# Performance work log

Measured on AMD Instinct MI355X. Metric: run time of the kernel, lower is better.

## Reference

```python
import jax, jax.numpy as jnp
import numpy as np

NEG_INF = jnp.finfo(jnp.float32).min


def _continual_mask(attach_test_after, Q, K, test_num, chunk_size):
    """Boolean allowed-mask [B, 1, Q, K] replicating get_continual_mask +
    the per-batch test-query/train-key override in forward()."""
    k_train = K - test_num * chunk_size
    q_train = Q - test_num * chunk_size
    qi = jnp.arange(Q)[:, None]          # [Q,1]
    kj = jnp.arange(K)[None, :]          # [1,K]
    # base causal mask with diagonal offset K-Q (train queries)
    base = kj <= qi + (K - Q)            # [Q,K]
    # block-diagonal tril for test-query / test-key region
    dq = qi - q_train                    # local test row (negative for train rows, unused there)
    dk = kj - k_train
    block = (kj >= k_train) & (dk <= dq) & ((dk // chunk_size) == (dq // chunk_size))
    # per-batch: test query in chunk n may see train keys <= attach_test_after[b, n]
    chunk_idx = jnp.clip(dq[:, 0], 0, None) // chunk_size          # [Q]
    att = attach_test_after[:, chunk_idx]                          # [B,Q]
    train_key_allowed = kj[None, :, :] <= att[:, :, None]          # [B,Q,K]
    allowed = jnp.where(qi < q_train, base[None],
                        jnp.where(kj[None] < k_train, train_key_allowed, block[None]))
    return allowed[:, None]              # [B,1,Q,K]


def setup_inputs() -> dict:
    key = jax.random.key(0)
    k1, k2, k3, k4 = jax.random.split(key, 4)
    B, L, H, D = 4, 2048, 8, 64
    test_num, train_len = 64, 1536
    return {
        "queries": jax.random.normal(k1, (B, L, H, D), dtype=jnp.float32),
        "keys": jax.random.normal(k2, (B, L, H, D), dtype=jnp.float32),
        "values": jax.random.normal(k3, (B, L, H, D), dtype=jnp.float32),
        "attach_test_after": jax.random.randint(k4, (B, test_num), 0, train_len).astype(jnp.int64),
        "train_len": train_len,
    }


def reference(queries, keys, values, attach_test_after, train_len):
    B, Lq, H, Dqk = queries.shape
    test_num = attach_test_after.shape[1]
    chunk_size = (Lq - train_len) // test_num
    q = jnp.transpose(queries, (0, 2, 1, 3))   # [B,H,Lq,D]
    k = jnp.transpose(keys, (0, 2, 1, 3))      # [B,H,Lk,D]
    v = jnp.transpose(values, (0, 2, 1, 3))    # [B,H,Lk,Dv]
    Lk = k.shape[2]
    # vanilla path: scaled QK^T + continual mask + softmax + AV
    logits = jnp.einsum('bhmd,bhnd->bhmn', q, k) / jnp.sqrt(jnp.float32(Dqk))
    allowed = _continual_mask(attach_test_after, Lq, Lk, test_num, chunk_size)
    logits = jnp.where(allowed, logits, NEG_INF)
    attn = jax.nn.softmax(logits, axis=-1)
    out = jnp.einsum('bhmn,bhnd->bhmd', attn, v)
    return out.transpose(0, 2, 1, 3).reshape(B, Lq, H * v.shape[-1])  # b l (h d)
```

## Files before the change

### kernel.cpp

```cpp
#include <hip/hip_runtime.h>
#include <hip/hip_bf16.h>

typedef __bf16 bf16_t;
typedef __bf16 bf16x8 __attribute__((ext_vector_type(8)));
typedef float  f32x4  __attribute__((ext_vector_type(4)));

#define MFMA16(a, b, c) __builtin_amdgcn_mfma_f32_16x16x32_bf16((a), (b), (c), 0, 0, 0)

constexpr int Bc = 4, Lc = 2048, Hc = 8, Dc = 64;
constexpr int HD = Hc * Dc;
constexpr int TRAINc = 1536;
constexpr int ROWS_BLK = 64;
constexpr int KT = 64;

constexpr int PREPK_BLOCKS = (int)((size_t)Bc * Lc * Hc * Dc / 8 / 256);

__global__ void prep_fused(const float* __restrict__ K, bf16_t* __restrict__ Kb,
                           const float* __restrict__ V, bf16_t* __restrict__ Vt) {
  __shared__ bf16_t T[64][64];
  const int t = (int)threadIdx.x;

  if ((int)blockIdx.x < PREPK_BLOCKS) {
    size_t g = ((size_t)blockIdx.x * 256 + t) * 8;
    float4 a = *(const float4*)(K + g);
    float4 b = *(const float4*)(K + g + 4);
    bf16x8 v;
    v[0] = (bf16_t)a.x; v[1] = (bf16_t)a.y; v[2] = (bf16_t)a.z; v[3] = (bf16_t)a.w;
    v[4] = (bf16_t)b.x; v[5] = (bf16_t)b.y; v[6] = (bf16_t)b.z; v[7] = (bf16_t)b.w;
    *(bf16x8*)(Kb + g) = v;
    return;
  }

  const int bid = (int)blockIdx.x - PREPK_BLOCKS;
  const int kt = bid & 31, h = (bid >> 5) & 7, b = bid >> 8;
  {
    int kl = t >> 2, dp = (t & 3) << 4;
    const float* s = V + ((size_t)(b * Lc + kt * 64 + kl) * Hc + h) * Dc + dp;
    bf16x8 v0, v1;
    float4 f;
    f = *(const float4*)(s);      v0[0]=(bf16_t)f.x; v0[1]=(bf16_t)f.y; v0[2]=(bf16_t)f.z; v0[3]=(bf16_t)f.w;
    f = *(const float4*)(s + 4);  v0[4]=(bf16_t)f.x; v0[5]=(bf16_t)f.y; v0[6]=(bf16_t)f.z; v0[7]=(bf16_t)f.w;
    f = *(const float4*)(s + 8);  v1[0]=(bf16_t)f.x; v1[1]=(bf16_t)f.y; v1[2]=(bf16_t)f.z; v1[3]=(bf16_t)f.w;
    f = *(const float4*)(s + 12); v1[4]=(bf16_t)f.x; v1[5]=(bf16_t)f.y; v1[6]=(bf16_t)f.z; v1[7]=(bf16_t)f.w;
    const int x = kl >> 3;
    const int c0 = dp >> 3;
    *(bf16x8*)&T[kl][(c0 ^ x) << 3]       = v0;
    *(bf16x8*)&T[kl][((c0 + 1) ^ x) << 3] = v1;
  }
  __syncthreads();
  {
    int d = t >> 2, kp = (t & 3) << 4;
    const int xa = kp >> 3;
    const int xb = xa + 1;
    const int lo = d & 7, hi = d >> 3;
    const int x0 = ((hi ^ xa) << 3) + lo;
    const int x1 = ((hi ^ xb) << 3) + lo;
    bf16x8 o0, o1;
#pragma unroll
    for (int i = 0; i < 8; ++i) { o0[i] = T[kp + i][x0]; o1[i] = T[kp + 8 + i][x1]; }
    bf16_t* dst = Vt + ((size_t)((b * Hc + h) * Dc + d)) * Lc + kt * 64 + kp;
    *(bf16x8*)dst = o0;
    *(bf16x8*)(dst + 8) = o1;
  }
}

static __device__ __forceinline__ void load16(const bf16_t* g, bf16_t* l) {
  __builtin_amdgcn_global_load_lds(
      (const __attribute__((address_space(1))) unsigned int*)g,
      (__attribute__((address_space(3))) unsigned int*)l, 16, 0, 0);
}

static __device__ __forceinline__ bf16x8 mk8(unsigned w0, unsigned w1,
                                             unsigned w2, unsigned w3) {
  union { unsigned u[4]; bf16x8 v; } x;
  x.u[0] = w0; x.u[1] = w1; x.u[2] = w2; x.u[3] = w3;
  return x.v;
}

__global__ __launch_bounds__(256, 4)
void continual_attn(const float* __restrict__ Qg, const bf16_t* __restrict__ Kb,
                    const bf16_t* __restrict__ Vt, const int* __restrict__ ATT,
                    float* __restrict__ OUT)
{
  __shared__ __align__(16) bf16_t Klds[2][KT * 64];
  __shared__ __align__(16) bf16_t Vlds[2][Dc * KT];

  const int bid  = blockIdx.x;
  const int qblk = 31 - (bid >> 5);
  const int h    = bid & 7;
  const int b    = (bid >> 3) & 3;
  const int q0   = qblk * ROWS_BLK;

  const int tid  = (int)threadIdx.x;
  const int wave = tid >> 6;
  const int lane = tid & 63;
  const int quad = lane >> 4;
  const int col  = lane & 15;
  const int qw   = q0 + wave * 16;

  const size_t bhQ = (size_t)b * Lc * HD + (size_t)h * Dc;

  const int kr = tid >> 3;
  const bf16_t* ksrcA = Kb + bhQ + (size_t)kr * HD + (((tid & 7) ^ (kr & 7)) << 3);
  const bf16_t* vsrcA = Vt + ((size_t)((b * Hc + h) * Dc + kr)) * Lc + (((tid & 7) ^ (kr & 7)) << 3);
  const bf16_t* vsrcB = vsrcA + (size_t)32 * Lc;

  bf16x8 aq[2];
  {
    const float* qp = Qg + bhQ + (size_t)(qw + col) * HD + quad * 8;
    const float SC = 0.125f * 1.44269504f;
#pragma unroll
    for (int t = 0; t < 2; ++t) {
      float4 lo = *(const float4*)(qp + t * 32);
      float4 hi = *(const float4*)(qp + t * 32 + 4);
      bf16x8 v;
      v[0] = (bf16_t)(lo.x * SC); v[1] = (bf16_t)(lo.y * SC);
      v[2] = (bf16_t)(lo.z * SC); v[3] = (bf16_t)(lo.w * SC);
      v[4] = (bf16_t)(hi.x * SC); v[5] = (bf16_t)(hi.y * SC);
      v[6] = (bf16_t)(hi.z * SC); v[7] = (bf16_t)(hi.w * SC);
      aq[t] = v;
    }
  }

  const bool testblk = (q0 >= TRAINc);
  const int qi = qw + col;
  int kendL, cstartL;
  if (testblk) {
    kendL   = ATT[b * 64 + ((qi - TRAINc) >> 3)] + 1;
    cstartL = qi & ~7;
  } else {
    kendL   = qi + 1;
    cstartL = 0;
  }

  int ntA, ndiag, kfull_end;
  if (testblk) {
    int c0 = (q0 - TRAINc) >> 3;
    int amax = 0, amin = 0x7fffffff;
#pragma unroll
    for (int i = 0; i < 8; ++i) {
      int a = ATT[b * 64 + c0 + i];
      amax = (a > amax) ? a : amax;
      amin = (a < amin) ? a : amin;
    }
    ntA = (amax >> 6) + 1;
    ndiag = 1;
    kfull_end = amin + 1;
  } else {
    ntA = qblk + 1;
    ndiag = 0;
    kfull_end = q0 + 1;
  }
  const int ntot = ntA + ndiag;

  float ls[4] = {0.f, 0.f, 0.f, 0.f};
  f32x4 o[4] = {{0,0,0,0},{0,0,0,0},{0,0,0,0},{0,0,0,0}};

  const int cA = ((quad ^ (col & 7)) << 3);

  {
    bf16_t* kd = Klds[0];
    bf16_t* vd = Vlds[0];
    load16(ksrcA, kd + wave * 512);
    load16(ksrcA + (size_t)32 * HD, kd + 2048 + wave * 512);
    load16(vsrcA, vd + wave * 512);
    load16(vsrcB, vd + 2048 + wave * 512);
  }

  for (int ti = 0; ti < ntot; ++ti) {
    const int buf = ti & 1;
    __syncthreads();

    if (ti + 1 < ntot) {
      const int kn = (ti + 1 < ntA) ? (ti + 1) * KT : q0 + (ti + 1 - ntA) * KT;
      bf16_t* kd = Klds[1 - buf];
      bf16_t* vd = Vlds[1 - buf];
      load16(ksrcA + (size_t)kn * HD, kd + wave * 512);
      load16(ksrcA + (size_t)(kn + 32) * HD, kd + 2048 + wave * 512);
      load16(vsrcA + kn, vd + wave * 512);
      load16(vsrcB + kn, vd + 2048 + wave * 512);
    }

    const bf16_t* kb = Klds[buf];
    const bf16_t* vbuf = Vlds[buf];
    const int k0 = (ti < ntA) ? ti * KT : q0 + (ti - ntA) * KT;

    f32x4 sf[4] = {{0,0,0,0},{0,0,0,0},{0,0,0,0},{0,0,0,0}};
    __builtin_amdgcn_s_setprio(1);
#pragma unroll
    for (int kg = 0; kg < 4; ++kg) {
      const bf16_t* krow = kb + (kg * 16 + col) * 64;
      bf16x8 k0f = *(const bf16x8*)(krow + cA);
      bf16x8 k1f = *(const bf16x8*)(krow + (cA ^ 32));
      sf[kg] = MFMA16(k0f, aq[0], sf[kg]);
      sf[kg] = MFMA16(k1f, aq[1], sf[kg]);
    }
    __builtin_amdgcn_s_setprio(0);

    const int mode = (ti >= ntA) ? 2 : ((k0 + KT <= kfull_end) ? 0 : 1);
    if (mode == 1) {
#pragma unroll
      for (int kg = 0; kg < 4; ++kg) {
        const int kv = k0 + kg * 16 + quad * 4;
#pragma unroll
        for (int r = 0; r < 4; ++r)
          if (kv + r >= kendL) sf[kg][r] = -1e30f;
      }
    } else if (mode == 2) {
#pragma unroll
      for (int kg = 0; kg < 4; ++kg) {
        const int kv = k0 + kg * 16 + quad * 4;
#pragma unroll
        for (int r = 0; r < 4; ++r)
          if (kv + r < cstartL || kv + r > qi) sf[kg][r] = -1e30f;
      }
    }

    float pvv[4][4];
#pragma unroll
    for (int kg = 0; kg < 4; ++kg)
#pragma unroll
      for (int r = 0; r < 4; ++r) {
        float p = __builtin_amdgcn_exp2f(sf[kg][r]);
        pvv[kg][r] = p;
        ls[r] += p;
      }

    unsigned Dw[4][2];
#pragma unroll
    for (int kg = 0; kg < 4; ++kg)
#pragma unroll
      for (int d = 0; d < 2; ++d)
        asm("v_cvt_pk_bf16_f32 %0, %1, %2"
            : "=v"(Dw[kg][d]) : "v"(pvv[kg][2 * d]), "v"(pvv[kg][2 * d + 1]));

    unsigned a0 = Dw[0][0], b0 = Dw[1][0];
    asm volatile("v_permlane32_swap_b32 %0, %1" : "+v"(a0), "+v"(b0));
    asm volatile("v_permlane16_swap_b32 %0, %1" : "+v"(a0), "+v"(b0));
    unsigned a1 = Dw[0][1], b1 = Dw[1][1];
    asm volatile("v_permlane32_swap_b32 %0, %1" : "+v"(a1), "+v"(b1));
    asm volatile("v_permlane16_swap_b32 %0, %1" : "+v"(a1), "+v"(b1));
    unsigned a2 = Dw[2][0], b2 = Dw[3][0];
    asm volatile("v_permlane32_swap_b32 %0, %1" : "+v"(a2), "+v"(b2));
    asm volatile("v_permlane16_swap_b32 %0, %1" : "+v"(a2), "+v"(b2));
    unsigned a3 = Dw[2][1], b3 = Dw[3][1];
    asm volatile("v_permlane32_swap_b32 %0, %1" : "+v"(a3), "+v"(b3));
    asm volatile("v_permlane16_swap_b32 %0, %1" : "+v"(a3), "+v"(b3));

    bf16x8 pa0 = mk8(a0, a1, b0, b1);
    bf16x8 pa1 = mk8(a2, a3, b2, b3);

    __builtin_amdgcn_s_setprio(1);
#pragma unroll
    for (int t = 0; t < 4; ++t) {
      const bf16_t* vrow = vbuf + (t * 16 + col) * 64;
      bf16x8 v0 = *(const bf16x8*)(vrow + cA);
      bf16x8 v1 = *(const bf16x8*)(vrow + (cA ^ 32));
      o[t] = MFMA16(pa0, v0, o[t]);
      o[t] = MFMA16(pa1, v1, o[t]);
    }
    __builtin_amdgcn_s_setprio(0);
  }

  float rs = (ls[0] + ls[1]) + (ls[2] + ls[3]);
  rs += __shfl_xor(rs, 16);
  rs += __shfl_xor(rs, 32);
#pragma unroll
  for (int r = 0; r < 4; ++r) {
    float dr = __shfl(rs, quad * 4 + r);
    float inv = 1.f / dr;
    int qo = qw + quad * 4 + r;
    float* op = OUT + ((size_t)b * Lc + qo) * HD + (size_t)h * Dc + col;
    op[0]  = o[0][r] * inv;
    op[16] = o[1][r] * inv;
    op[32] = o[2][r] * inv;
    op[48] = o[3][r] * inv;
  }
}

extern "C" void kernel_launch(void* const* d_in, const int* in_sizes, int n_in,
                              void* d_out, int out_size, void* d_ws, size_t ws_size,
                              hipStream_t stream) {
  const float* Q   = (const float*)d_in[0];
  const float* K   = (const float*)d_in[1];
  const float* V   = (const float*)d_in[2];
  const int*   ATT = (const int*)d_in[3];
  float* OUT = (float*)d_out;
  (void)in_sizes; (void)n_in; (void)out_size; (void)ws_size;

  const size_t NE = (size_t)Bc * Lc * Hc * Dc;
  bf16_t* Kb = (bf16_t*)d_ws;
  bf16_t* Vt = Kb + NE;

  prep_fused<<<dim3((unsigned)(PREPK_BLOCKS + Bc * Hc * (Lc / 64))), dim3(256), 0, stream>>>(K, Kb, V, Vt);
  continual_attn<<<dim3(Bc * Hc * (Lc / ROWS_BLK)), dim3(256), 0, stream>>>(Q, Kb, Vt, ATT, OUT);
}
```

Before: 126.7 us.

## Load K/V tiles directly from global into registers, drop LDS staging

Replaces the double-buffered LDS staging of K and V tiles (global_load_lds plus block barriers) with per-wave direct global loads into registers feeding the MFMAs. It also reorders the q-block schedule so heavy and light causal blocks are interleaved across the grid. This removes LDS traffic and __syncthreads, but each of the four waves now fetches the same K/V data separately, and with no prefetch the load latency is exposed inside each iteration.

```diff
diff --git a/kernel.cpp b/kernel.cpp
--- a/kernel.cpp
+++ b/kernel.cpp
@@ -64,12 +64,6 @@
   }
 }
 
-static __device__ __forceinline__ void load16(const bf16_t* g, bf16_t* l) {
-  __builtin_amdgcn_global_load_lds(
-      (const __attribute__((address_space(1))) unsigned int*)g,
-      (__attribute__((address_space(3))) unsigned int*)l, 16, 0, 0);
-}
-
 static __device__ __forceinline__ bf16x8 mk8(unsigned w0, unsigned w1,
                                              unsigned w2, unsigned w3) {
   union { unsigned u[4]; bf16x8 v; } x;
@@ -82,11 +76,13 @@
                     const bf16_t* __restrict__ Vt, const int* __restrict__ ATT,
                     float* __restrict__ OUT)
 {
-  __shared__ __align__(16) bf16_t Klds[2][KT * 64];
-  __shared__ __align__(16) bf16_t Vlds[2][Dc * KT];
-
   const int bid  = blockIdx.x;
-  const int qblk = 31 - (bid >> 5);
+  const int g    = bid >> 5;
+  int qblk;
+  if (g < 8)       qblk = 24 + g;
+  else if (g < 16) qblk = 15 - g;
+  else if (g < 24) qblk = g - 8;
+  else             qblk = 47 - g;
   const int h    = bid & 7;
   const int b    = (bid >> 3) & 3;
   const int q0   = qblk * ROWS_BLK;
@@ -100,10 +96,8 @@
 
   const size_t bhQ = (size_t)b * Lc * HD + (size_t)h * Dc;
 
-  const int kr = tid >> 3;
-  const bf16_t* ksrcA = Kb + bhQ + (size_t)kr * HD + (((tid & 7) ^ (kr & 7)) << 3);
-  const bf16_t* vsrcA = Vt + ((size_t)((b * Hc + h) * Dc + kr)) * Lc + (((tid & 7) ^ (kr & 7)) << 3);
-  const bf16_t* vsrcB = vsrcA + (size_t)32 * Lc;
+  const bf16_t* kfb = Kb + bhQ + (size_t)col * HD + quad * 8;
+  const bf16_t* vfb = Vt + ((size_t)((b * Hc + h) * Dc) + col) * Lc + quad * 8;
 
   bf16x8 aq[2];
   {
@@ -156,44 +150,29 @@
   float ls[4] = {0.f, 0.f, 0.f, 0.f};
   f32x4 o[4] = {{0,0,0,0},{0,0,0,0},{0,0,0,0},{0,0,0,0}};
 
-  const int cA = ((quad ^ (col & 7)) << 3);
-
-  {
-    bf16_t* kd = Klds[0];
-    bf16_t* vd = Vlds[0];
-    load16(ksrcA, kd + wave * 512);
-    load16(ksrcA + (size_t)32 * HD, kd + 2048 + wave * 512);
-    load16(vsrcA, vd + wave * 512);
-    load16(vsrcB, vd + 2048 + wave * 512);
-  }
-
   for (int ti = 0; ti < ntot; ++ti) {
-    const int buf = ti & 1;
-    __syncthreads();
-
-    if (ti + 1 < ntot) {
-      const int kn = (ti + 1 < ntA) ? (ti + 1) * KT : q0 + (ti + 1 - ntA) * KT;
-      bf16_t* kd = Klds[1 - buf];
-      bf16_t* vd = Vlds[1 - buf];
-      load16(ksrcA + (size_t)kn * HD, kd + wave * 512);
-      load16(ksrcA + (size_t)(kn + 32) * HD, kd + 2048 + wave * 512);
-      load16(vsrcA + kn, vd + wave * 512);
-      load16(vsrcB + kn, vd + 2048 + wave * 512);
-    }
-
-    const bf16_t* kb = Klds[buf];
-    const bf16_t* vbuf = Vlds[buf];
     const int k0 = (ti < ntA) ? ti * KT : q0 + (ti - ntA) * KT;
+
+    bf16x8 kf0[4], kf1[4], vf0[4], vf1[4];
+#pragma unroll
+    for (int kg = 0; kg < 4; ++kg) {
+      const bf16_t* p = kfb + (size_t)(k0 + kg * 16) * HD;
+      kf0[kg] = *(const bf16x8*)p;
+      kf1[kg] = *(const bf16x8*)(p + 32);
+    }
+#pragma unroll
+    for (int t = 0; t < 4; ++t) {
+      const bf16_t* p = vfb + (size_t)(t * 16) * Lc + k0;
+      vf0[t] = *(const bf16x8*)p;
+      vf1[t] = *(const bf16x8*)(p + 32);
+    }
 
     f32x4 sf[4] = {{0,0,0,0},{0,0,0,0},{0,0,0,0},{0,0,0,0}};
     __builtin_amdgcn_s_setprio(1);
 #pragma unroll
     for (int kg = 0; kg < 4; ++kg) {
-      const bf16_t* krow = kb + (kg * 16 + col) * 64;
-      bf16x8 k0f = *(const bf16x8*)(krow + cA);
-      bf16x8 k1f = *(const bf16x8*)(krow + (cA ^ 32));
-      sf[kg] = MFMA16(k0f, aq[0], sf[kg]);
-      sf[kg] = MFMA16(k1f, aq[1], sf[kg]);
+      sf[kg] = MFMA16(kf0[kg], aq[0], sf[kg]);
+      sf[kg] = MFMA16(kf1[kg], aq[1], sf[kg]);
     }
     __builtin_amdgcn_s_setprio(0);
 
@@ -253,11 +232,8 @@
     __builtin_amdgcn_s_setprio(1);
 #pragma unroll
     for (int t = 0; t < 4; ++t) {
-      const bf16_t* vrow = vbuf + (t * 16 + col) * 64;
-      bf16x8 v0 = *(const bf16x8*)(vrow + cA);
-      bf16x8 v1 = *(const bf16x8*)(vrow + (cA ^ 32));
-      o[t] = MFMA16(pa0, v0, o[t]);
-      o[t] = MFMA16(pa1, v1, o[t]);
+      o[t] = MFMA16(pa0, vf0[t], o[t]);
+      o[t] = MFMA16(pa1, vf1[t], o[t]);
     }
     __builtin_amdgcn_s_setprio(0);
   }
```

Measured after the change: 214.1 us. +69.0%, slower.

## Software-pipeline QK^T one tile ahead and reorder query-block scheduling

Applied to the files above, without the earlier changes.

Restructures the attention loop so the QK^T MFMAs and masking for tile ti+1 are issued before the softmax/exp and PV MFMAs of tile ti, with K prefetched two tiles ahead and V one tile ahead. The goal is to overlap the exp/convert/permlane work with matrix instructions and to hide load latency. It also changes the block-to-query-block mapping into a zigzag order so heavy and light causal blocks are interleaved for better load balance. The cost is more live registers (two score sets), some redundant loads and MFMAs at the loop tail from the clamped tile index, and the setprio around QK^T is dropped.

```diff
diff --git a/kernel.cpp b/kernel.cpp
--- a/kernel.cpp
+++ b/kernel.cpp
@@ -86,7 +86,12 @@
   __shared__ __align__(16) bf16_t Vlds[2][Dc * KT];
 
   const int bid  = blockIdx.x;
-  const int qblk = 31 - (bid >> 5);
+  const int g    = bid >> 5;
+  int qblk;
+  if (g < 8)       qblk = 24 + g;
+  else if (g < 16) qblk = 15 - g;
+  else if (g < 24) qblk = g - 8;
+  else             qblk = 47 - g;
   const int h    = bid & 7;
   const int b    = (bid >> 3) & 3;
   const int q0   = qblk * ROWS_BLK;
@@ -158,35 +163,28 @@
 
   const int cA = ((quad ^ (col & 7)) << 3);
 
-  {
-    bf16_t* kd = Klds[0];
-    bf16_t* vd = Vlds[0];
-    load16(ksrcA, kd + wave * 512);
-    load16(ksrcA + (size_t)32 * HD, kd + 2048 + wave * 512);
-    load16(vsrcA, vd + wave * 512);
-    load16(vsrcB, vd + 2048 + wave * 512);
-  }
-
-  for (int ti = 0; ti < ntot; ++ti) {
-    const int buf = ti & 1;
-    __syncthreads();
-
-    if (ti + 1 < ntot) {
-      const int kn = (ti + 1 < ntA) ? (ti + 1) * KT : q0 + (ti + 1 - ntA) * KT;
-      bf16_t* kd = Klds[1 - buf];
-      bf16_t* vd = Vlds[1 - buf];
-      load16(ksrcA + (size_t)kn * HD, kd + wave * 512);
-      load16(ksrcA + (size_t)(kn + 32) * HD, kd + 2048 + wave * 512);
-      load16(vsrcA + kn, vd + wave * 512);
-      load16(vsrcB + kn, vd + 2048 + wave * 512);
-    }
-
-    const bf16_t* kb = Klds[buf];
-    const bf16_t* vbuf = Vlds[buf];
-    const int k0 = (ti < ntA) ? ti * KT : q0 + (ti - ntA) * KT;
-
+  auto tk0 = [&](int t) {
+    int tc = (t < ntot) ? t : (ntot - 1);
+    return (tc < ntA) ? tc * KT : q0 + (tc - ntA) * KT;
+  };
+
+  {
+    load16(ksrcA, Klds[0] + wave * 512);
+    load16(ksrcA + (size_t)32 * HD, Klds[0] + 2048 + wave * 512);
+  }
+  __syncthreads();
+  {
+    const int k1p = tk0(1);
+    load16(vsrcA, Vlds[0] + wave * 512);
+    load16(vsrcB, Vlds[0] + 2048 + wave * 512);
+    load16(ksrcA + (size_t)k1p * HD, Klds[1] + wave * 512);
+    load16(ksrcA + (size_t)(k1p + 32) * HD, Klds[1] + 2048 + wave * 512);
+  }
+
+  f32x4 sfA[4];
+  {
+    const bf16_t* kb = Klds[0];
     f32x4 sf[4] = {{0,0,0,0},{0,0,0,0},{0,0,0,0},{0,0,0,0}};
-    __builtin_amdgcn_s_setprio(1);
 #pragma unroll
     for (int kg = 0; kg < 4; ++kg) {
       const bf16_t* krow = kb + (kg * 16 + col) * 64;
@@ -195,33 +193,81 @@
       sf[kg] = MFMA16(k0f, aq[0], sf[kg]);
       sf[kg] = MFMA16(k1f, aq[1], sf[kg]);
     }
-    __builtin_amdgcn_s_setprio(0);
-
-    const int mode = (ti >= ntA) ? 2 : ((k0 + KT <= kfull_end) ? 0 : 1);
-    if (mode == 1) {
+    const int mode0 = (0 >= ntA) ? 2 : ((KT <= kfull_end) ? 0 : 1);
+    if (mode0 == 1) {
 #pragma unroll
       for (int kg = 0; kg < 4; ++kg) {
-        const int kv = k0 + kg * 16 + quad * 4;
+        const int kv = kg * 16 + quad * 4;
 #pragma unroll
         for (int r = 0; r < 4; ++r)
           if (kv + r >= kendL) sf[kg][r] = -1e30f;
       }
-    } else if (mode == 2) {
+    } else if (mode0 == 2) {
 #pragma unroll
       for (int kg = 0; kg < 4; ++kg) {
-        const int kv = k0 + kg * 16 + quad * 4;
+        const int kv = kg * 16 + quad * 4;
 #pragma unroll
         for (int r = 0; r < 4; ++r)
           if (kv + r < cstartL || kv + r > qi) sf[kg][r] = -1e30f;
       }
     }
+#pragma unroll
+    for (int i = 0; i < 4; ++i) sfA[i] = sf[i];
+  }
+
+  for (int ti = 0; ti < ntot; ++ti) {
+    __syncthreads();
+
+    {
+      const int k2 = tk0(ti + 2);
+      const int k1 = tk0(ti + 1);
+      bf16_t* kd = Klds[ti & 1];
+      bf16_t* vd = Vlds[(ti + 1) & 1];
+      load16(ksrcA + (size_t)k2 * HD, kd + wave * 512);
+      load16(ksrcA + (size_t)(k2 + 32) * HD, kd + 2048 + wave * 512);
+      load16(vsrcA + k1, vd + wave * 512);
+      load16(vsrcB + k1, vd + 2048 + wave * 512);
+    }
+
+    f32x4 sfB[4] = {{0,0,0,0},{0,0,0,0},{0,0,0,0},{0,0,0,0}};
+    {
+      const int t1 = (ti + 1 < ntot) ? ti + 1 : ntot - 1;
+      const int k1 = tk0(ti + 1);
+      const bf16_t* kb = Klds[(ti + 1) & 1];
+#pragma unroll
+      for (int kg = 0; kg < 4; ++kg) {
+        const bf16_t* krow = kb + (kg * 16 + col) * 64;
+        bf16x8 k0f = *(const bf16x8*)(krow + cA);
+        bf16x8 k1f = *(const bf16x8*)(krow + (cA ^ 32));
+        sfB[kg] = MFMA16(k0f, aq[0], sfB[kg]);
+        sfB[kg] = MFMA16(k1f, aq[1], sfB[kg]);
+      }
+      const int mode = (t1 >= ntA) ? 2 : ((k1 + KT <= kfull_end) ? 0 : 1);
+      if (mode == 1) {
+#pragma unroll
+        for (int kg = 0; kg < 4; ++kg) {
+          const int kv = k1 + kg * 16 + quad * 4;
+#pragma unroll
+          for (int r = 0; r < 4; ++r)
+            if (kv + r >= kendL) sfB[kg][r] = -1e30f;
+        }
+      } else if (mode == 2) {
+#pragma unroll
+        for (int kg = 0; kg < 4; ++kg) {
+          const int kv = k1 + kg * 16 + quad * 4;
+#pragma unroll
+          for (int r = 0; r < 4; ++r)
+            if (kv + r < cstartL || kv + r > qi) sfB[kg][r] = -1e30f;
+        }
+      }
+    }
 
     float pvv[4][4];
 #pragma unroll
     for (int kg = 0; kg < 4; ++kg)
 #pragma unroll
       for (int r = 0; r < 4; ++r) {
-        float p = __builtin_amdgcn_exp2f(sf[kg][r]);
+        float p = __builtin_amdgcn_exp2f(sfA[kg][r]);
         pvv[kg][r] = p;
         ls[r] += p;
       }
@@ -250,6 +296,7 @@
     bf16x8 pa0 = mk8(a0, a1, b0, b1);
     bf16x8 pa1 = mk8(a2, a3, b2, b3);
 
+    const bf16_t* vbuf = Vlds[ti & 1];
     __builtin_amdgcn_s_setprio(1);
 #pragma unroll
     for (int t = 0; t < 4; ++t) {
@@ -260,6 +307,9 @@
       o[t] = MFMA16(pa1, v1, o[t]);
     }
     __builtin_amdgcn_s_setprio(0);
+
+#pragma unroll
+    for (int i = 0; i < 4; ++i) sfA[i] = sfB[i];
   }
 
   float rs = (ls[0] + ls[1]) + (ls[2] + ls[3]);
```

After: 129.1 us. Within noise of the previous version (+1.9%).

## Split key tiles across two wave groups per block and merge partial outputs

Applied to the files above, without the earlier changes.

Doubles the block to 512 threads so two groups of four waves each process half of the key tiles for the same 64 query rows, with separate double-buffered LDS. The partial output accumulators and row sums are combined through shared memory before normalization and store. Block scheduling order is also changed so test-region blocks (rows 1536+) go first. This shortens the serial key loop per block to fix the long-tail imbalance of causal rows, at the cost of doubled LDS per block, an extra reduction step, and padded dummy tiles when the tile count is odd.

```diff
diff --git a/kernel.cpp b/kernel.cpp
--- a/kernel.cpp
+++ b/kernel.cpp
@@ -77,32 +77,35 @@
   return x.v;
 }
 
-__global__ __launch_bounds__(256, 4)
+__global__ __launch_bounds__(512, 4)
 void continual_attn(const float* __restrict__ Qg, const bf16_t* __restrict__ Kb,
                     const bf16_t* __restrict__ Vt, const int* __restrict__ ATT,
                     float* __restrict__ OUT)
 {
-  __shared__ __align__(16) bf16_t Klds[2][KT * 64];
-  __shared__ __align__(16) bf16_t Vlds[2][Dc * KT];
+  __shared__ __align__(16) bf16_t Klds[2][2][KT * 64];
+  __shared__ __align__(16) bf16_t Vlds[2][2][Dc * KT];
 
   const int bid  = blockIdx.x;
-  const int qblk = 31 - (bid >> 5);
+  const int g    = bid >> 5;
+  const int qblk = (g < 8) ? 24 + g : 31 - g;
   const int h    = bid & 7;
   const int b    = (bid >> 3) & 3;
   const int q0   = qblk * ROWS_BLK;
 
   const int tid  = (int)threadIdx.x;
-  const int wave = tid >> 6;
+  const int sub  = tid >> 8;
+  const int stid = tid & 255;
+  const int w4   = (tid >> 6) & 3;
   const int lane = tid & 63;
   const int quad = lane >> 4;
   const int col  = lane & 15;
-  const int qw   = q0 + wave * 16;
+  const int qw   = q0 + w4 * 16;
 
   const size_t bhQ = (size_t)b * Lc * HD + (size_t)h * Dc;
 
-  const int kr = tid >> 3;
-  const bf16_t* ksrcA = Kb + bhQ + (size_t)kr * HD + (((tid & 7) ^ (kr & 7)) << 3);
-  const bf16_t* vsrcA = Vt + ((size_t)((b * Hc + h) * Dc + kr)) * Lc + (((tid & 7) ^ (kr & 7)) << 3);
+  const int kr = stid >> 3;
+  const bf16_t* ksrcA = Kb + bhQ + (size_t)kr * HD + (((stid & 7) ^ (kr & 7)) << 3);
+  const bf16_t* vsrcA = Vt + ((size_t)((b * Hc + h) * Dc + kr)) * Lc + (((stid & 7) ^ (kr & 7)) << 3);
   const bf16_t* vsrcB = vsrcA + (size_t)32 * Lc;
 
   bf16x8 aq[2];
@@ -152,38 +155,46 @@
     kfull_end = q0 + 1;
   }
   const int ntot = ntA + ndiag;
+  const int nh   = (ntot + 1) >> 1;
 
   float ls[4] = {0.f, 0.f, 0.f, 0.f};
   f32x4 o[4] = {{0,0,0,0},{0,0,0,0},{0,0,0,0},{0,0,0,0}};
 
   const int cA = ((quad ^ (col & 7)) << 3);
 
+  auto tkk = [&](int t) {
+    int tc = (t < ntot) ? t : (ntot - 1);
+    return (tc < ntA) ? tc * KT : q0 + (tc - ntA) * KT;
+  };
+
   {
-    bf16_t* kd = Klds[0];
-    bf16_t* vd = Vlds[0];
-    load16(ksrcA, kd + wave * 512);
-    load16(ksrcA + (size_t)32 * HD, kd + 2048 + wave * 512);
-    load16(vsrcA, vd + wave * 512);
-    load16(vsrcB, vd + 2048 + wave * 512);
-  }
-
-  for (int ti = 0; ti < ntot; ++ti) {
+    const int kp = tkk(sub * nh);
+    bf16_t* kd = Klds[sub][0];
+    bf16_t* vd = Vlds[sub][0];
+    load16(ksrcA + (size_t)kp * HD, kd + w4 * 512);
+    load16(ksrcA + (size_t)(kp + 32) * HD, kd + 2048 + w4 * 512);
+    load16(vsrcA + kp, vd + w4 * 512);
+    load16(vsrcB + kp, vd + 2048 + w4 * 512);
+  }
+
+  for (int ti = 0; ti < nh; ++ti) {
     const int buf = ti & 1;
+    const int myt = sub * nh + ti;
     __syncthreads();
 
-    if (ti + 1 < ntot) {
-      const int kn = (ti + 1 < ntA) ? (ti + 1) * KT : q0 + (ti + 1 - ntA) * KT;
-      bf16_t* kd = Klds[1 - buf];
-      bf16_t* vd = Vlds[1 - buf];
-      load16(ksrcA + (size_t)kn * HD, kd + wave * 512);
-      load16(ksrcA + (size_t)(kn + 32) * HD, kd + 2048 + wave * 512);
-      load16(vsrcA + kn, vd + wave * 512);
-      load16(vsrcB + kn, vd + 2048 + wave * 512);
-    }
-
-    const bf16_t* kb = Klds[buf];
-    const bf16_t* vbuf = Vlds[buf];
-    const int k0 = (ti < ntA) ? ti * KT : q0 + (ti - ntA) * KT;
+    if (ti + 1 < nh) {
+      const int kn = tkk(myt + 1);
+      bf16_t* kd = Klds[sub][1 - buf];
+      bf16_t* vd = Vlds[sub][1 - buf];
+      load16(ksrcA + (size_t)kn * HD, kd + w4 * 512);
+      load16(ksrcA + (size_t)(kn + 32) * HD, kd + 2048 + w4 * 512);
+      load16(vsrcA + kn, vd + w4 * 512);
+      load16(vsrcB + kn, vd + 2048 + w4 * 512);
+    }
+
+    const bf16_t* kb = Klds[sub][buf];
+    const bf16_t* vbuf = Vlds[sub][buf];
+    const int k0 = tkk(myt);
 
     f32x4 sf[4] = {{0,0,0,0},{0,0,0,0},{0,0,0,0},{0,0,0,0}};
     __builtin_amdgcn_s_setprio(1);
@@ -197,22 +208,29 @@
     }
     __builtin_amdgcn_s_setprio(0);
 
-    const int mode = (ti >= ntA) ? 2 : ((k0 + KT <= kfull_end) ? 0 : 1);
-    if (mode == 1) {
-#pragma unroll
-      for (int kg = 0; kg < 4; ++kg) {
-        const int kv = k0 + kg * 16 + quad * 4;
-#pragma unroll
-        for (int r = 0; r < 4; ++r)
-          if (kv + r >= kendL) sf[kg][r] = -1e30f;
-      }
-    } else if (mode == 2) {
-#pragma unroll
-      for (int kg = 0; kg < 4; ++kg) {
-        const int kv = k0 + kg * 16 + quad * 4;
-#pragma unroll
-        for (int r = 0; r < 4; ++r)
-          if (kv + r < cstartL || kv + r > qi) sf[kg][r] = -1e30f;
+    if (myt >= ntot) {
+#pragma unroll
+      for (int kg = 0; kg < 4; ++kg)
+#pragma unroll
+        for (int r = 0; r < 4; ++r) sf[kg][r] = -1e30f;
+    } else {
+      const int mode = (myt >= ntA) ? 2 : ((k0 + KT <= kfull_end) ? 0 : 1);
+      if (mode == 1) {
+#pragma unroll
+        for (int kg = 0; kg < 4; ++kg) {
+          const int kv = k0 + kg * 16 + quad * 4;
+#pragma unroll
+          for (int r = 0; r < 4; ++r)
+            if (kv + r >= kendL) sf[kg][r] = -1e30f;
+        }
+      } else if (mode == 2) {
+#pragma unroll
+        for (int kg = 0; kg < 4; ++kg) {
+          const int kv = k0 + kg * 16 + quad * 4;
+#pragma unroll
+          for (int r = 0; r < 4; ++r)
+            if (kv + r < cstartL || kv + r > qi) sf[kg][r] = -1e30f;
+        }
       }
     }
 
@@ -265,16 +283,37 @@
   float rs = (ls[0] + ls[1]) + (ls[2] + ls[3]);
   rs += __shfl_xor(rs, 16);
   rs += __shfl_xor(rs, 32);
-#pragma unroll
-  for (int r = 0; r < 4; ++r) {
-    float dr = __shfl(rs, quad * 4 + r);
-    float inv = 1.f / dr;
-    int qo = qw + quad * 4 + r;
-    float* op = OUT + ((size_t)b * Lc + qo) * HD + (size_t)h * Dc + col;
-    op[0]  = o[0][r] * inv;
-    op[16] = o[1][r] * inv;
-    op[32] = o[2][r] * inv;
-    op[48] = o[3][r] * inv;
+
+  __syncthreads();
+  float* M = (float*)&Klds[0][0][0];
+  if (sub == 1) {
+    float* m = M + ((size_t)(w4 * 64 + lane)) * 20;
+    *(f32x4*)(m + 0)  = o[0];
+    *(f32x4*)(m + 4)  = o[1];
+    *(f32x4*)(m + 8)  = o[2];
+    *(f32x4*)(m + 12) = o[3];
+    m[16] = rs;
+  }
+  __syncthreads();
+  if (sub == 0) {
+    const float* m = M + ((size_t)(w4 * 64 + lane)) * 20;
+    o[0] += *(const f32x4*)(m + 0);
+    o[1] += *(const f32x4*)(m + 4);
+    o[2] += *(const f32x4*)(m + 8);
+    o[3] += *(const f32x4*)(m + 12);
+    rs += m[16];
+
+#pragma unroll
+    for (int r = 0; r < 4; ++r) {
+      float dr = __shfl(rs, quad * 4 + r);
+      float inv = 1.f / dr;
+      int qo = qw + quad * 4 + r;
+      float* op = OUT + ((size_t)b * Lc + qo) * HD + (size_t)h * Dc + col;
+      op[0]  = o[0][r] * inv;
+      op[16] = o[1][r] * inv;
+      op[32] = o[2][r] * inv;
+      op[48] = o[3][r] * inv;
+    }
   }
 }
 
@@ -293,5 +332,5 @@
   bf16_t* Vt = Kb + NE;
 
   prep_fused<<<dim3((unsigned)(PREPK_BLOCKS + Bc * Hc * (Lc / 64))), dim3(256), 0, stream>>>(K, Kb, V, Vt);
-  continual_attn<<<dim3(Bc * Hc * (Lc / ROWS_BLK)), dim3(256), 0, stream>>>(Q, Kb, Vt, ATT, OUT);
-}
+  continual_attn<<<dim3(Bc * Hc * (Lc / ROWS_BLK)), dim3(512), 0, stream>>>(Q, Kb, Vt, ATT, OUT);
+}
```

Measured after the change: 129.4 us. 2.2% more time.
